# Optimization experiments

Hardware: AMD Instinct MI355X
Metric: run time of the kernel (lower is better)

Reference implementation:

```python
import jax, jax.numpy as jnp
import numpy as np

DIM = 1024
HEADS = 16
HEAD_DIM = DIM // HEADS
B, N, S = 4, 4096, 512


def setup_inputs() -> dict:
    key = jax.random.key(0)
    ks = jax.random.split(key, 9)
    scale = DIM ** -0.5
    return {
        "x": jax.random.normal(ks[0], (B, N, DIM), dtype=jnp.float32),
        "context": jax.random.normal(ks[1], (B, S, DIM), dtype=jnp.float32),
        "context_mask": jax.random.uniform(ks[2], (B, S)) < 0.2,  # True = padding
        "q_w": jax.random.normal(ks[3], (DIM, DIM), dtype=jnp.float32) * scale,
        "q_b": jnp.zeros((DIM,), dtype=jnp.float32),
        "kv_w": jax.random.normal(ks[4], (DIM, 2 * DIM), dtype=jnp.float32) * scale,
        "kv_b": jnp.zeros((2 * DIM,), dtype=jnp.float32),
        "proj_w": jax.random.normal(ks[5], (DIM, DIM), dtype=jnp.float32) * scale,
        "proj_b": jnp.zeros((DIM,), dtype=jnp.float32),
    }


def reference(x, context, context_mask, q_w, q_b, kv_w, kv_b, proj_w, proj_b):
    b, n, c = x.shape
    s = context.shape[1]
    h, d = HEADS, HEAD_DIM
    scale = d ** -0.5

    # projections
    q = (x @ q_w + q_b).reshape(b, n, h, d)            # [B,N,H,D]
    kv = (context @ kv_w + kv_b).reshape(b, s, 2, h, d)
    k = kv[:, :, 0]                                     # [B,S,H,D]
    v = kv[:, :, 1]

    # scores [B,H,N,S]
    attn = jnp.einsum("bnhd,bshd->bhns", q, k) * scale
    attn = jnp.where(context_mask[:, None, None, :], -jnp.inf, attn)
    attn = jax.nn.softmax(attn, axis=-1)

    out = jnp.einsum("bhns,bshd->bnhd", attn, v).reshape(b, n, c)
    return out @ proj_w + proj_b
```

## Files before the change

kernel.cpp:

```cpp
#include <hip/hip_runtime.h>
#include <hip/hip_bf16.h>

typedef __attribute__((ext_vector_type(8))) short bf16x8;
typedef __attribute__((ext_vector_type(4))) float f32x4;
typedef unsigned short u16;

#define DIMC 1024
#define NHEAD 16
#define HDIM 64
#define NB 4
#define NQ 4096
#define NS 512

#define LOG2E 1.44269504f

#if __has_builtin(__builtin_amdgcn_exp2f)
#define EXP2F(x) __builtin_amdgcn_exp2f(x)
#else
#define EXP2F(x) __expf(0.69314718f * (x))
#endif

#if __has_builtin(__builtin_amdgcn_rcpf)
#define RCPF(x) __builtin_amdgcn_rcpf(x)
#else
#define RCPF(x) (1.0f / (x))
#endif

__device__ __forceinline__ u16 f2bf(float f) {
  __hip_bfloat16 h = __float2bfloat16(f);
  return *reinterpret_cast<u16*>(&h);
}

__device__ __forceinline__ unsigned pack_bf2(float a, float b) {
  __hip_bfloat162 h2 = __float22bfloat162_rn(make_float2(a, b));
  return *reinterpret_cast<unsigned*>(&h2);
}

__device__ __forceinline__ void gload_lds16(const void* g, void* s) {
  __builtin_amdgcn_global_load_lds(
      (const __attribute__((address_space(1))) void*)g,
      (__attribute__((address_space(3))) void*)s, 16, 0, 0);
}


__device__ __forceinline__ void cvt_body(const float* __restrict__ in,
                                         u16* __restrict__ out, int base, int nblk,
                                         int n4) {
  const int stride = nblk * 256;
  for (int i = base * 256 + threadIdx.x; i < n4; i += stride) {
    float4 v = *(const float4*)(in + (size_t)i * 4);
    ushort4 o;
    o.x = f2bf(v.x); o.y = f2bf(v.y); o.z = f2bf(v.z); o.w = f2bf(v.w);
    *(ushort4*)(out + (size_t)i * 4) = o;
  }
}

__global__ void prep_kernel(const float* __restrict__ x, const float* __restrict__ ctx,
                            const int* __restrict__ cmask,
                            const float* __restrict__ q_w, const float* __restrict__ kv_w,
                            const float* __restrict__ proj_w,
                            u16* __restrict__ x_bf, u16* __restrict__ ctx_bf,
                            u16* __restrict__ qwT, u16* __restrict__ kvwT,
                            u16* __restrict__ pwT, float* __restrict__ maskf) {
  __shared__ float t[32][33];
  const int bid = blockIdx.x;
  if (bid < 2048) {
    cvt_body(x, x_bf, bid, 2048, 16777216 / 4);
    return;
  }
  if (bid < 2560) {
    cvt_body(ctx, ctx_bf, bid - 2048, 512, 2097152 / 4);
    return;
  }
  if (bid >= 6656) {
    const int i = (bid - 6656) * 256 + threadIdx.x;
    if (i < NB * NS) maskf[i] = cmask[i] ? -1e30f : 0.0f;
    return;
  }
  const float* W;
  u16* WT;
  int K, N, local;
  if (bid < 3584) {
    W = q_w; WT = qwT; K = 1024; N = 1024; local = bid - 2560;
  } else if (bid < 5632) {
    W = kv_w; WT = kvwT; K = 1024; N = 2048; local = bid - 3584;
  } else {
    W = proj_w; WT = pwT; K = 1024; N = 1024; local = bid - 5632;
  }
  const int nbx = N >> 5;
  const int bx = (local % nbx) * 32;
  const int by = (local / nbx) * 32;
  const int tx = threadIdx.x & 31, ty = threadIdx.x >> 5;
#pragma unroll
  for (int i = 0; i < 32; i += 8)
    t[ty + i][tx] = W[(size_t)(by + ty + i) * N + bx + tx];
  __syncthreads();
#pragma unroll
  for (int i = 0; i < 32; i += 8)
    WT[(size_t)(bx + ty + i) * K + by + tx] = f2bf(t[tx][ty + i]);
}


__launch_bounds__(256)
__global__ void gemm_kv(const u16* __restrict__ A, const u16* __restrict__ BT,
                        const float* __restrict__ bias, u16* __restrict__ Kout,
                        u16* __restrict__ VTout, int M, int N, int K) {
  __shared__ __align__(16) u16 As[128 * 32];
  __shared__ __align__(16) u16 Bs[128 * 32];
  const int tid = threadIdx.x;
  const int w = tid >> 6, l = tid & 63;
  const int wr = w >> 1, wc = w & 1;
  const int fr = l & 15, fhi = l >> 4;

  const int nwg = gridDim.x * gridDim.y;
  const int o = blockIdx.y * gridDim.x + blockIdx.x;
  const int tIdx = (o & 7) * (nwg >> 3) + (o >> 3);
  const int m0 = (tIdx / gridDim.x) * 128;
  const int n0 = (tIdx % gridDim.x) * 128;

  const f32x4 fz = {0.f, 0.f, 0.f, 0.f};
  f32x4 acc[4][4];
#pragma unroll
  for (int mt = 0; mt < 4; mt++)
#pragma unroll
    for (int nt = 0; nt < 4; nt++) acc[mt][nt] = fz;

  const int f0 = w * 2048 + l * 16;
  const int f1 = f0 + 1024;
  const int ar0 = f0 >> 6, ac0 = (f0 & 63) >> 1;
  const int ar1 = f1 >> 6, ac1 = (f1 & 63) >> 1;
  const u16* Ag0 = A + (size_t)(m0 + ar0) * K + ac0;
  const u16* Ag1 = A + (size_t)(m0 + ar1) * K + ac1;
  const u16* Bg0 = BT + (size_t)(n0 + ar0) * K + ac0;
  const u16* Bg1 = BT + (size_t)(n0 + ar1) * K + ac1;

  for (int k0 = 0; k0 < K; k0 += 32) {
    gload_lds16(Ag0 + k0, &As[w * 1024]);
    gload_lds16(Ag1 + k0, &As[w * 1024 + 512]);
    gload_lds16(Bg0 + k0, &Bs[w * 1024]);
    gload_lds16(Bg1 + k0, &Bs[w * 1024 + 512]);
    __syncthreads();

    bf16x8 a[4], b[4];
#pragma unroll
    for (int t = 0; t < 4; t++) {
      a[t] = *(const bf16x8*)&As[(wr * 64 + t * 16 + fr) * 32 + fhi * 8];
      b[t] = *(const bf16x8*)&Bs[(wc * 64 + t * 16 + fr) * 32 + fhi * 8];
    }
#pragma unroll
    for (int mt = 0; mt < 4; mt++)
#pragma unroll
      for (int nt = 0; nt < 4; nt++)
        acc[mt][nt] = __builtin_amdgcn_mfma_f32_16x16x32_bf16(a[mt], b[nt], acc[mt][nt], 0, 0, 0);
    __syncthreads();
  }

#pragma unroll
  for (int mt = 0; mt < 4; mt++) {
#pragma unroll
    for (int nt = 0; nt < 4; nt++) {
      const int col = n0 + wc * 64 + nt * 16 + fr;
      const float bv = bias[col];
#pragma unroll
      for (int r = 0; r < 4; r++) {
        const int row = m0 + wr * 64 + mt * 16 + fhi * 4 + r;
        const float v = acc[mt][nt][r] + bv;
        const int b = row >> 9, s = row & 511;
        if (col < 1024) {
          const int h = col >> 6, d = col & 63;
          Kout[(((size_t)(b * 16 + h)) * 512 + s) * 64 + d] = f2bf(v);
        } else {
          const int c2 = col - 1024;
          const int h = c2 >> 6, d = c2 & 63;
          VTout[(((size_t)(b * 16 + h)) * 64 + d) * 512 + s] = f2bf(v);
        }
      }
    }
  }
}


template<int MODE>
__launch_bounds__(512, 1)
__global__ void gemm256(const u16* __restrict__ A, const u16* __restrict__ BT,
                        const float* __restrict__ bias, void* __restrict__ C0,
                        int M, int N, int K) {
  __shared__ __align__(16) u16 As[2][16384];
  __shared__ __align__(16) u16 Bs[2][16384];
  const int tid = threadIdx.x;
  const int w = tid >> 6, l = tid & 63;
  const int wm = w >> 2, wn = w & 3;
  const int fr = l & 15, fhi = l >> 4;

  const int nblk = gridDim.x;
  const int nN = N >> 8;
  const int o = blockIdx.x;
  const int tIdx = (o & 7) * (nblk >> 3) + (o >> 3);
  const int m0 = (tIdx / nN) << 8;
  const int n0 = (tIdx % nN) << 8;

  const int rowoff = tid >> 3;
  const int gchunk = (tid & 7) ^ (rowoff & 7);
  const u16* Abase = A + (size_t)(m0 + rowoff) * K + gchunk * 8;
  const u16* Bbase = BT + (size_t)(n0 + rowoff) * K + gchunk * 8;
  const int ldsoff = w * 512;

  const f32x4 fz = {0.f, 0.f, 0.f, 0.f};
  f32x4 acc[2][4][4];
#pragma unroll
  for (int mh = 0; mh < 2; mh++)
#pragma unroll
    for (int m = 0; m < 4; m++)
#pragma unroll
      for (int n = 0; n < 4; n++) acc[mh][m][n] = fz;

  const int KT = K >> 6;

#pragma unroll
  for (int p = 0; p < 4; ++p) {
    gload_lds16(Abase + (size_t)(p * 64) * K, &As[0][p * 4096 + ldsoff]);
    gload_lds16(Bbase + (size_t)(p * 64) * K, &Bs[0][p * 4096 + ldsoff]);
  }
  asm volatile("s_waitcnt vmcnt(0)" ::: "memory");
  __builtin_amdgcn_s_barrier();

  int nb = 0;
  for (int kt = 0; kt < KT; ++kt) {
    const int knext = (kt + 1) << 6;
    const bool more = (kt + 1) < KT;
#pragma unroll
    for (int p = 0; p < 4; ++p) {
      const int mh = p >> 1, kk = p & 1;
      const int ch = ((kk << 2) | fhi) ^ (fr & 7);
      bf16x8 af[4], bfr[4];
#pragma unroll
      for (int m = 0; m < 4; ++m) {
        const int row = wm * 128 + mh * 64 + m * 16 + fr;
        af[m] = *(const bf16x8*)((const char*)&As[nb][0] + row * 128 + ch * 16);
      }
#pragma unroll
      for (int n = 0; n < 4; ++n) {
        const int row = wn * 64 + n * 16 + fr;
        bfr[n] = *(const bf16x8*)((const char*)&Bs[nb][0] + row * 128 + ch * 16);
      }
      if (more) {
        gload_lds16(Abase + (size_t)(p * 64) * K + knext, &As[nb ^ 1][p * 4096 + ldsoff]);
        gload_lds16(Bbase + (size_t)(p * 64) * K + knext, &Bs[nb ^ 1][p * 4096 + ldsoff]);
      }
      __builtin_amdgcn_s_barrier();
      asm volatile("s_waitcnt lgkmcnt(0)" ::: "memory");
      __builtin_amdgcn_s_setprio(1);
#pragma unroll
      for (int m = 0; m < 4; ++m)
#pragma unroll
        for (int n = 0; n < 4; ++n)
          acc[mh][m][n] = __builtin_amdgcn_mfma_f32_16x16x32_bf16(af[m], bfr[n], acc[mh][m][n], 0, 0, 0);
      __builtin_amdgcn_s_setprio(0);
      __builtin_amdgcn_s_barrier();
    }
    asm volatile("s_waitcnt vmcnt(0)" ::: "memory");
    __builtin_amdgcn_s_barrier();
    nb ^= 1;
  }

#pragma unroll
  for (int mh = 0; mh < 2; ++mh)
#pragma unroll
    for (int m = 0; m < 4; ++m)
#pragma unroll
      for (int n = 0; n < 4; ++n) {
        const int col = n0 + wn * 64 + n * 16 + fr;
        const float bv = bias[col];
#pragma unroll
        for (int r = 0; r < 4; ++r) {
          const int row = m0 + wm * 128 + mh * 64 + m * 16 + fhi * 4 + r;
          const float v = acc[mh][m][n][r] + bv;
          if (MODE == 0)
            ((u16*)C0)[(size_t)row * N + col] = f2bf(v * 0.125f);
          else
            ((float*)C0)[(size_t)row * N + col] = v;
        }
      }
}

__launch_bounds__(512, 2)
__global__ void attn_kernel(const u16* __restrict__ Q, const u16* __restrict__ Kb,
                            const u16* __restrict__ VT, const float* __restrict__ maskf,
                            u16* __restrict__ O) {
  __shared__ __align__(16) u16 Ks[512 * 64];
  __shared__ __align__(16) u16 Vs[64 * 512];
  __shared__ __align__(16) u16 Ps[8][2048];
  const int tid = threadIdx.x, w = tid >> 6, l = tid & 63;
  const int fr = l & 15, fhi = l >> 4;

  const int rid = blockIdx.x;
  const int orig = ((rid & 7) << 6) + (rid >> 3);
  const int bh = orig >> 3, qc = orig & 7;
  const int b = bh >> 4, h = bh & 15;

  const u16* Kg = Kb + (size_t)bh * NS * HDIM;
  const u16* Vg = VT + (size_t)bh * HDIM * NS;
  const float* mrow = maskf + b * NS;

#pragma unroll
  for (int it = 0; it < 8; ++it) {
    const int slot = it * 512 + tid;
    const int r = slot >> 3, c3 = slot & 7;
    const int gc = c3 ^ (r & 7);
    gload_lds16(Kg + (size_t)r * HDIM + gc * 8, &Ks[slot * 8]);
  }
#pragma unroll
  for (int it = 0; it < 8; ++it) {
    const int slot = it * 512 + tid;
    const int r = slot >> 6, c6 = slot & 63;
    const int gc = c6 ^ (r & 7);
    gload_lds16(Vg + (size_t)r * NS + gc * 8, &Vs[slot * 8]);
  }
  asm volatile("s_waitcnt vmcnt(0)" ::: "memory");
  __syncthreads();

  u16* Pw = Ps[w];
  const f32x4 fz = {0.f, 0.f, 0.f, 0.f};

#pragma unroll 1
  for (int qt = 0; qt < 2; ++qt) {
    const int rowbase = b * NQ + qc * 512 + w * 64 + qt * 32;

    bf16x8 qf[2][2];
#pragma unroll
    for (int mt = 0; mt < 2; mt++)
#pragma unroll
      for (int kk = 0; kk < 2; kk++)
        qf[mt][kk] = *(const bf16x8*)&Q[(size_t)(rowbase + mt * 16 + fr) * DIMC +
                                        h * 64 + kk * 32 + fhi * 8];

    float l_run[2] = {0.f, 0.f};
    f32x4 o_acc[2][4];
#pragma unroll
    for (int mt = 0; mt < 2; mt++)
#pragma unroll
      for (int dn = 0; dn < 4; dn++) o_acc[mt][dn] = fz;

#pragma unroll
    for (int t = 0; t < 8; ++t) {
      const int sc = t * 64;

      f32x4 sacc[2][4];
#pragma unroll
      for (int mt = 0; mt < 2; mt++)
#pragma unroll
        for (int sn = 0; sn < 4; sn++) sacc[mt][sn] = fz;

      __builtin_amdgcn_s_setprio(1);
#pragma unroll
      for (int kk = 0; kk < 2; kk++) {
        bf16x8 kf[4];
#pragma unroll
        for (int sn = 0; sn < 4; sn++) {
          const int row = sc + sn * 16 + fr;
          const int byte = row * 128 + ((((kk << 2) | fhi) ^ (fr & 7)) << 4);
          kf[sn] = *(const bf16x8*)((const char*)&Ks[0] + byte);
        }
#pragma unroll
        for (int sn = 0; sn < 4; sn++)
#pragma unroll
          for (int mt = 0; mt < 2; mt++)
            sacc[mt][sn] = __builtin_amdgcn_mfma_f32_16x16x32_bf16(kf[sn], qf[mt][kk], sacc[mt][sn], 0, 0, 0);
      }
      __builtin_amdgcn_s_setprio(0);

      float4 mv4[4];
#pragma unroll
      for (int sn = 0; sn < 4; sn++)
        mv4[sn] = *(const float4*)&mrow[sc + sn * 16 + fhi * 4];

#pragma unroll
      for (int mt = 0; mt < 2; mt++) {
        float ls = 0.f;
        const int qrow = mt * 16 + fr;
#pragma unroll
        for (int sn = 0; sn < 4; sn++) {
          const float e0 = EXP2F(fmaf(sacc[mt][sn][0], LOG2E, ((const float*)&mv4[sn])[0]));
          const float e1 = EXP2F(fmaf(sacc[mt][sn][1], LOG2E, ((const float*)&mv4[sn])[1]));
          const float e2 = EXP2F(fmaf(sacc[mt][sn][2], LOG2E, ((const float*)&mv4[sn])[2]));
          const float e3 = EXP2F(fmaf(sacc[mt][sn][3], LOG2E, ((const float*)&mv4[sn])[3]));
          ls += (e0 + e1) + (e2 + e3);
          int byte = qrow * 128 + sn * 32 + fhi * 8;
          byte ^= (qrow & 7) << 4;
          uint2 pk;
          pk.x = pack_bf2(e0, e1);
          pk.y = pack_bf2(e2, e3);
          *(uint2*)((char*)Pw + byte) = pk;
        }
        l_run[mt] += ls;
      }
      asm volatile("s_waitcnt lgkmcnt(0)" ::: "memory");

      __builtin_amdgcn_s_setprio(1);
#pragma unroll
      for (int kk = 0; kk < 2; kk++) {
        bf16x8 vv[4];
#pragma unroll
        for (int dn = 0; dn < 4; dn++) {
          const int row = dn * 16 + fr;
          const int byte = row * 1024 +
              (((sc >> 3) + ((((kk << 2) | fhi) ^ (fr & 7)))) << 4);
          vv[dn] = *(const bf16x8*)((const char*)&Vs[0] + byte);
        }
#pragma unroll
        for (int mt = 0; mt < 2; mt++) {
          int byte = (mt * 16 + fr) * 128 + kk * 64 + fhi * 16;
          byte ^= (fr & 7) << 4;
          const bf16x8 pa = *(const bf16x8*)((char*)Pw + byte);
#pragma unroll
          for (int dn = 0; dn < 4; dn++)
            o_acc[mt][dn] = __builtin_amdgcn_mfma_f32_16x16x32_bf16(pa, vv[dn], o_acc[mt][dn], 0, 0, 0);
        }
      }
      __builtin_amdgcn_s_setprio(0);
    }

#pragma unroll
    for (int mt = 0; mt < 2; mt++) {
      l_run[mt] += __shfl_xor(l_run[mt], 16);
      l_run[mt] += __shfl_xor(l_run[mt], 32);
    }
#pragma unroll
    for (int mt = 0; mt < 2; mt++) {
      float lo[4];
#pragma unroll
      for (int r = 0; r < 4; r++) {
        lo[r] = RCPF(__shfl(l_run[mt], fhi * 4 + r));
      }
#pragma unroll
      for (int dn = 0; dn < 4; dn++)
#pragma unroll
        for (int r = 0; r < 4; r++) {
          const float v = o_acc[mt][dn][r] * lo[r];
          const int row = rowbase + mt * 16 + fhi * 4 + r;
          O[(size_t)row * DIMC + h * 64 + dn * 16 + fr] = f2bf(v);
        }
    }
  }
}


extern "C" void kernel_launch(void* const* d_in, const int* in_sizes, int n_in,
                              void* d_out, int out_size, void* d_ws, size_t ws_size,
                              hipStream_t stream) {
  const float* x      = (const float*)d_in[0];
  const float* ctx    = (const float*)d_in[1];
  const int*   cmask  = (const int*)d_in[2];
  const float* q_w    = (const float*)d_in[3];
  const float* q_b    = (const float*)d_in[4];
  const float* kv_w   = (const float*)d_in[5];
  const float* kv_b   = (const float*)d_in[6];
  const float* proj_w = (const float*)d_in[7];
  const float* proj_b = (const float*)d_in[8];
  float* out = (float*)d_out;

  char* ws = (char*)d_ws;
  size_t off = 0;
  auto alloc = [&](size_t bytes) {
    void* p = ws + off;
    off += (bytes + 255) & ~(size_t)255;
    return p;
  };
  u16* x_bf   = (u16*)alloc((size_t)16384 * 1024 * 2);
  u16* ctx_bf = (u16*)alloc((size_t)2048 * 1024 * 2);
  u16* qwT    = (u16*)alloc((size_t)1024 * 1024 * 2);
  u16* kvwT   = (u16*)alloc((size_t)2048 * 1024 * 2);
  u16* pwT    = (u16*)alloc((size_t)1024 * 1024 * 2);
  u16* Qb     = (u16*)alloc((size_t)16384 * 1024 * 2);
  u16* Kbuf   = (u16*)alloc((size_t)64 * 512 * 64 * 2);
  u16* VTbuf  = (u16*)alloc((size_t)64 * 64 * 512 * 2);
  u16* Ob     = (u16*)alloc((size_t)16384 * 1024 * 2);
  float* maskf = (float*)alloc((size_t)NB * NS * 4);

  prep_kernel<<<6664, 256, 0, stream>>>(x, ctx, cmask, q_w, kv_w, proj_w,
                                        x_bf, ctx_bf, qwT, kvwT, pwT, maskf);

  gemm256<0><<<256, 512, 0, stream>>>(x_bf, qwT, q_b, Qb, 16384, 1024, 1024);
  gemm_kv<<<dim3(16, 16), 256, 0, stream>>>(ctx_bf, kvwT, kv_b, Kbuf, VTbuf, 2048, 2048, 1024);
  attn_kernel<<<512, 512, 0, stream>>>(Qb, Kbuf, VTbuf, maskf, Ob);
  gemm256<2><<<256, 512, 0, stream>>>(Ob, pwT, proj_b, out, 16384, 1024, 1024);
}
```

Baseline: 182.5 us.

## Interleave two query sub-tiles per wave to overlap softmax with MFMA

The attention kernel used to walk its two 32-row query sub-tiles one after the other. It now keeps both sub-tiles live and interleaves them inside each key chunk: it computes QK for sub-tile A, runs A's exp, computes QK for B, runs A's PV, then B's exp and B's PV. The aim is to hide the exp/pack work and the LDS round-trip behind independent MFMA work and to share the mask loads. In exchange the register footprint roughly doubles (two sets of Q fragments, score and output accumulators), which risks lower occupancy or spills. The single P buffer is also reused between the two sub-tiles, which depends on the lgkmcnt waits for correct ordering.

```diff
diff --git a/kernel.cpp b/kernel.cpp
--- a/kernel.cpp
+++ b/kernel.cpp
@@ -322,125 +322,197 @@
   u16* Pw = Ps[w];
   const f32x4 fz = {0.f, 0.f, 0.f, 0.f};
 
-#pragma unroll 1
-  for (int qt = 0; qt < 2; ++qt) {
-    const int rowbase = b * NQ + qc * 512 + w * 64 + qt * 32;
-
-    bf16x8 qf[2][2];
+  const int rowbase_a = b * NQ + qc * 512 + w * 64;
+  const int rowbase_b = rowbase_a + 32;
+
+  bf16x8 qfa[2][2], qfb[2][2];
+#pragma unroll
+  for (int mt = 0; mt < 2; mt++)
+#pragma unroll
+    for (int kk = 0; kk < 2; kk++) {
+      qfa[mt][kk] = *(const bf16x8*)&Q[(size_t)(rowbase_a + mt * 16 + fr) * DIMC +
+                                       h * 64 + kk * 32 + fhi * 8];
+      qfb[mt][kk] = *(const bf16x8*)&Q[(size_t)(rowbase_b + mt * 16 + fr) * DIMC +
+                                       h * 64 + kk * 32 + fhi * 8];
+    }
+
+  float l_a[2] = {0.f, 0.f}, l_b[2] = {0.f, 0.f};
+  f32x4 oa[2][4], ob[2][4];
+#pragma unroll
+  for (int mt = 0; mt < 2; mt++)
+#pragma unroll
+    for (int dn = 0; dn < 4; dn++) { oa[mt][dn] = fz; ob[mt][dn] = fz; }
+
+#pragma unroll
+  for (int t = 0; t < 8; ++t) {
+    const int sc = t * 64;
+
+    float4 mv4[4];
+#pragma unroll
+    for (int sn = 0; sn < 4; sn++)
+      mv4[sn] = *(const float4*)&mrow[sc + sn * 16 + fhi * 4];
+
+    f32x4 sa[2][4];
 #pragma unroll
     for (int mt = 0; mt < 2; mt++)
 #pragma unroll
-      for (int kk = 0; kk < 2; kk++)
-        qf[mt][kk] = *(const bf16x8*)&Q[(size_t)(rowbase + mt * 16 + fr) * DIMC +
-                                        h * 64 + kk * 32 + fhi * 8];
-
-    float l_run[2] = {0.f, 0.f};
-    f32x4 o_acc[2][4];
+      for (int sn = 0; sn < 4; sn++) sa[mt][sn] = fz;
+    __builtin_amdgcn_s_setprio(1);
+#pragma unroll
+    for (int kk = 0; kk < 2; kk++) {
+      bf16x8 kf[4];
+#pragma unroll
+      for (int sn = 0; sn < 4; sn++) {
+        const int row = sc + sn * 16 + fr;
+        const int byte = row * 128 + ((((kk << 2) | fhi) ^ (fr & 7)) << 4);
+        kf[sn] = *(const bf16x8*)((const char*)&Ks[0] + byte);
+      }
+#pragma unroll
+      for (int sn = 0; sn < 4; sn++)
+#pragma unroll
+        for (int mt = 0; mt < 2; mt++)
+          sa[mt][sn] = __builtin_amdgcn_mfma_f32_16x16x32_bf16(kf[sn], qfa[mt][kk], sa[mt][sn], 0, 0, 0);
+    }
+    __builtin_amdgcn_s_setprio(0);
+
+#pragma unroll
+    for (int mt = 0; mt < 2; mt++) {
+      float ls = 0.f;
+      const int qrow = mt * 16 + fr;
+#pragma unroll
+      for (int sn = 0; sn < 4; sn++) {
+        const float e0 = EXP2F(fmaf(sa[mt][sn][0], LOG2E, ((const float*)&mv4[sn])[0]));
+        const float e1 = EXP2F(fmaf(sa[mt][sn][1], LOG2E, ((const float*)&mv4[sn])[1]));
+        const float e2 = EXP2F(fmaf(sa[mt][sn][2], LOG2E, ((const float*)&mv4[sn])[2]));
+        const float e3 = EXP2F(fmaf(sa[mt][sn][3], LOG2E, ((const float*)&mv4[sn])[3]));
+        ls += (e0 + e1) + (e2 + e3);
+        int byte = qrow * 128 + sn * 32 + fhi * 8;
+        byte ^= (qrow & 7) << 4;
+        uint2 pk;
+        pk.x = pack_bf2(e0, e1);
+        pk.y = pack_bf2(e2, e3);
+        *(uint2*)((char*)Pw + byte) = pk;
+      }
+      l_a[mt] += ls;
+    }
+
+    f32x4 sb[2][4];
 #pragma unroll
     for (int mt = 0; mt < 2; mt++)
 #pragma unroll
-      for (int dn = 0; dn < 4; dn++) o_acc[mt][dn] = fz;
-
-#pragma unroll
-    for (int t = 0; t < 8; ++t) {
-      const int sc = t * 64;
-
-      f32x4 sacc[2][4];
-#pragma unroll
-      for (int mt = 0; mt < 2; mt++)
-#pragma unroll
-        for (int sn = 0; sn < 4; sn++) sacc[mt][sn] = fz;
-
-      __builtin_amdgcn_s_setprio(1);
-#pragma unroll
-      for (int kk = 0; kk < 2; kk++) {
-        bf16x8 kf[4];
-#pragma unroll
-        for (int sn = 0; sn < 4; sn++) {
-          const int row = sc + sn * 16 + fr;
-          const int byte = row * 128 + ((((kk << 2) | fhi) ^ (fr & 7)) << 4);
-          kf[sn] = *(const bf16x8*)((const char*)&Ks[0] + byte);
-        }
-#pragma unroll
-        for (int sn = 0; sn < 4; sn++)
-#pragma unroll
-          for (int mt = 0; mt < 2; mt++)
-            sacc[mt][sn] = __builtin_amdgcn_mfma_f32_16x16x32_bf16(kf[sn], qf[mt][kk], sacc[mt][sn], 0, 0, 0);
-      }
-      __builtin_amdgcn_s_setprio(0);
-
-      float4 mv4[4];
+      for (int sn = 0; sn < 4; sn++) sb[mt][sn] = fz;
+    __builtin_amdgcn_s_setprio(1);
+#pragma unroll
+    for (int kk = 0; kk < 2; kk++) {
+      bf16x8 kf[4];
+#pragma unroll
+      for (int sn = 0; sn < 4; sn++) {
+        const int row = sc + sn * 16 + fr;
+        const int byte = row * 128 + ((((kk << 2) | fhi) ^ (fr & 7)) << 4);
+        kf[sn] = *(const bf16x8*)((const char*)&Ks[0] + byte);
+      }
 #pragma unroll
       for (int sn = 0; sn < 4; sn++)
-        mv4[sn] = *(const float4*)&mrow[sc + sn * 16 + fhi * 4];
-
+#pragma unroll
+        for (int mt = 0; mt < 2; mt++)
+          sb[mt][sn] = __builtin_amdgcn_mfma_f32_16x16x32_bf16(kf[sn], qfb[mt][kk], sb[mt][sn], 0, 0, 0);
+    }
+    __builtin_amdgcn_s_setprio(0);
+
+    asm volatile("s_waitcnt lgkmcnt(0)" ::: "memory");
+    __builtin_amdgcn_s_setprio(1);
+#pragma unroll
+    for (int kk = 0; kk < 2; kk++) {
+      bf16x8 vv[4];
+#pragma unroll
+      for (int dn = 0; dn < 4; dn++) {
+        const int row = dn * 16 + fr;
+        const int byte = row * 1024 +
+            (((sc >> 3) + ((((kk << 2) | fhi) ^ (fr & 7)))) << 4);
+        vv[dn] = *(const bf16x8*)((const char*)&Vs[0] + byte);
+      }
 #pragma unroll
       for (int mt = 0; mt < 2; mt++) {
-        float ls = 0.f;
-        const int qrow = mt * 16 + fr;
-#pragma unroll
-        for (int sn = 0; sn < 4; sn++) {
-          const float e0 = EXP2F(fmaf(sacc[mt][sn][0], LOG2E, ((const float*)&mv4[sn])[0]));
-          const float e1 = EXP2F(fmaf(sacc[mt][sn][1], LOG2E, ((const float*)&mv4[sn])[1]));
-          const float e2 = EXP2F(fmaf(sacc[mt][sn][2], LOG2E, ((const float*)&mv4[sn])[2]));
-          const float e3 = EXP2F(fmaf(sacc[mt][sn][3], LOG2E, ((const float*)&mv4[sn])[3]));
-          ls += (e0 + e1) + (e2 + e3);
-          int byte = qrow * 128 + sn * 32 + fhi * 8;
-          byte ^= (qrow & 7) << 4;
-          uint2 pk;
-          pk.x = pack_bf2(e0, e1);
-          pk.y = pack_bf2(e2, e3);
-          *(uint2*)((char*)Pw + byte) = pk;
-        }
-        l_run[mt] += ls;
-      }
-      asm volatile("s_waitcnt lgkmcnt(0)" ::: "memory");
-
-      __builtin_amdgcn_s_setprio(1);
-#pragma unroll
-      for (int kk = 0; kk < 2; kk++) {
-        bf16x8 vv[4];
-#pragma unroll
-        for (int dn = 0; dn < 4; dn++) {
-          const int row = dn * 16 + fr;
-          const int byte = row * 1024 +
-              (((sc >> 3) + ((((kk << 2) | fhi) ^ (fr & 7)))) << 4);
-          vv[dn] = *(const bf16x8*)((const char*)&Vs[0] + byte);
-        }
-#pragma unroll
-        for (int mt = 0; mt < 2; mt++) {
-          int byte = (mt * 16 + fr) * 128 + kk * 64 + fhi * 16;
-          byte ^= (fr & 7) << 4;
-          const bf16x8 pa = *(const bf16x8*)((char*)Pw + byte);
-#pragma unroll
-          for (int dn = 0; dn < 4; dn++)
-            o_acc[mt][dn] = __builtin_amdgcn_mfma_f32_16x16x32_bf16(pa, vv[dn], o_acc[mt][dn], 0, 0, 0);
-        }
-      }
-      __builtin_amdgcn_s_setprio(0);
-    }
+        int byte = (mt * 16 + fr) * 128 + kk * 64 + fhi * 16;
+        byte ^= (fr & 7) << 4;
+        const bf16x8 pa = *(const bf16x8*)((char*)Pw + byte);
+#pragma unroll
+        for (int dn = 0; dn < 4; dn++)
+          oa[mt][dn] = __builtin_amdgcn_mfma_f32_16x16x32_bf16(pa, vv[dn], oa[mt][dn], 0, 0, 0);
+      }
+    }
+    __builtin_amdgcn_s_setprio(0);
 
 #pragma unroll
     for (int mt = 0; mt < 2; mt++) {
-      l_run[mt] += __shfl_xor(l_run[mt], 16);
-      l_run[mt] += __shfl_xor(l_run[mt], 32);
-    }
-#pragma unroll
-    for (int mt = 0; mt < 2; mt++) {
-      float lo[4];
+      float ls = 0.f;
+      const int qrow = mt * 16 + fr;
+#pragma unroll
+      for (int sn = 0; sn < 4; sn++) {
+        const float e0 = EXP2F(fmaf(sb[mt][sn][0], LOG2E, ((const float*)&mv4[sn])[0]));
+        const float e1 = EXP2F(fmaf(sb[mt][sn][1], LOG2E, ((const float*)&mv4[sn])[1]));
+        const float e2 = EXP2F(fmaf(sb[mt][sn][2], LOG2E, ((const float*)&mv4[sn])[2]));
+        const float e3 = EXP2F(fmaf(sb[mt][sn][3], LOG2E, ((const float*)&mv4[sn])[3]));
+        ls += (e0 + e1) + (e2 + e3);
+        int byte = qrow * 128 + sn * 32 + fhi * 8;
+        byte ^= (qrow & 7) << 4;
+        uint2 pk;
+        pk.x = pack_bf2(e0, e1);
+        pk.y = pack_bf2(e2, e3);
+        *(uint2*)((char*)Pw + byte) = pk;
+      }
+      l_b[mt] += ls;
+    }
+
+    asm volatile("s_waitcnt lgkmcnt(0)" ::: "memory");
+    __builtin_amdgcn_s_setprio(1);
+#pragma unroll
+    for (int kk = 0; kk < 2; kk++) {
+      bf16x8 vv[4];
+#pragma unroll
+      for (int dn = 0; dn < 4; dn++) {
+        const int row = dn * 16 + fr;
+        const int byte = row * 1024 +
+            (((sc >> 3) + ((((kk << 2) | fhi) ^ (fr & 7)))) << 4);
+        vv[dn] = *(const bf16x8*)((const char*)&Vs[0] + byte);
+      }
+#pragma unroll
+      for (int mt = 0; mt < 2; mt++) {
+        int byte = (mt * 16 + fr) * 128 + kk * 64 + fhi * 16;
+        byte ^= (fr & 7) << 4;
+        const bf16x8 pa = *(const bf16x8*)((char*)Pw + byte);
+#pragma unroll
+        for (int dn = 0; dn < 4; dn++)
+          ob[mt][dn] = __builtin_amdgcn_mfma_f32_16x16x32_bf16(pa, vv[dn], ob[mt][dn], 0, 0, 0);
+      }
+    }
+    __builtin_amdgcn_s_setprio(0);
+  }
+
+#pragma unroll
+  for (int mt = 0; mt < 2; mt++) {
+    l_a[mt] += __shfl_xor(l_a[mt], 16);
+    l_a[mt] += __shfl_xor(l_a[mt], 32);
+    l_b[mt] += __shfl_xor(l_b[mt], 16);
+    l_b[mt] += __shfl_xor(l_b[mt], 32);
+  }
+#pragma unroll
+  for (int mt = 0; mt < 2; mt++) {
+    float loa[4], lob[4];
+#pragma unroll
+    for (int r = 0; r < 4; r++) {
+      loa[r] = RCPF(__shfl(l_a[mt], fhi * 4 + r));
+      lob[r] = RCPF(__shfl(l_b[mt], fhi * 4 + r));
+    }
+#pragma unroll
+    for (int dn = 0; dn < 4; dn++)
 #pragma unroll
       for (int r = 0; r < 4; r++) {
-        lo[r] = RCPF(__shfl(l_run[mt], fhi * 4 + r));
-      }
-#pragma unroll
-      for (int dn = 0; dn < 4; dn++)
-#pragma unroll
-        for (int r = 0; r < 4; r++) {
-          const float v = o_acc[mt][dn][r] * lo[r];
-          const int row = rowbase + mt * 16 + fhi * 4 + r;
-          O[(size_t)row * DIMC + h * 64 + dn * 16 + fr] = f2bf(v);
-        }
-    }
+        const int rowa = rowbase_a + mt * 16 + fhi * 4 + r;
+        O[(size_t)rowa * DIMC + h * 64 + dn * 16 + fr] = f2bf(oa[mt][dn][r] * loa[r]);
+        const int rowb = rowbase_b + mt * 16 + fhi * 4 + r;
+        O[(size_t)rowb * DIMC + h * 64 + dn * 16 + fr] = f2bf(ob[mt][dn][r] * lob[r]);
+      }
   }
 }
 
```

New measurement: 184.8 us. About the same (+1.3%).
